# Performance work log

Hardware: AMD Instinct MI355X
Metric: run time of the kernel (lower is better)

The kernel has to match this reference:

```python
import jax, jax.numpy as jnp
import numpy as np

N = 1024  # feature_size == hidden_size == n_nodes
K = 3     # diffusion hops
B = 2048  # batch


def setup_inputs() -> dict:
    key = jax.random.key(0)
    ks = jax.random.split(key, 32)

    # --- adjacency -> normalized K-hop filter list (constants in torch, requires_grad=False) ---
    A = jax.random.uniform(ks[0], (N, N), dtype=jnp.float32) + jnp.eye(N, dtype=jnp.float32)
    # D_inverse = diag(1/sum(A, 0)); norm_A = D_inverse @ A  -> row i scaled by 1/colsum[i]
    norm_A = A / jnp.sum(A, axis=0)[:, None]
    A_temp = jnp.eye(N, dtype=jnp.float32)
    hops = []
    for _ in range(K):
        A_temp = jnp.minimum(A_temp @ norm_A, 1.0)  # Clamp_A: clamp(max=1.0)
        hops.append(A_temp)
    A_list = jnp.stack(hops)  # [K, N, N]

    stdv = 1.0 / np.sqrt(N)
    gin = K * N + 2 * N  # gc_input_size + hidden*2
    rin = N + 2 * N      # input_size + hidden*2

    def U(k, shape, fan_in):
        s = 1.0 / np.sqrt(fan_in)
        return jax.random.uniform(k, shape, jnp.float32, -s, s)

    inp = {
        "input": jax.random.normal(ks[1], (B, N), jnp.float32),
        "input_t": jax.random.normal(ks[2], (B, N), jnp.float32),
        "Hidden_State": jax.random.normal(ks[3], (B, N), jnp.float32),
        "Cell_State": jax.random.normal(ks[4], (B, N), jnp.float32),
        "rHidden_State": jax.random.normal(ks[5], (B, N), jnp.float32),
        "rCell_State": jax.random.normal(ks[6], (B, N), jnp.float32),
        "pred": jax.random.normal(ks[7], (B, N), jnp.float32),
        "A_list": A_list,
        "gc_W": U(ks[8], (K, N, N), N),  # FilterLinear weights (masked by A_list)
        "fl_W": U(ks[9], (N, gin), gin), "fl_b": U(ks[10], (N,), gin),
        "il_W": U(ks[11], (N, gin), gin), "il_b": U(ks[12], (N,), gin),
        "ol_W": U(ks[13], (N, gin), gin), "ol_b": U(ks[14], (N,), gin),
        "Cl_W": U(ks[15], (N, gin), gin), "Cl_b": U(ks[16], (N,), gin),
        "Neighbor_weight": jax.random.uniform(ks[17], (N,), jnp.float32, -stdv, stdv),
        "rfl_W": U(ks[18], (N, rin), rin), "rfl_b": U(ks[19], (N,), rin),
        "ril_W": U(ks[20], (N, rin), rin), "ril_b": U(ks[21], (N,), rin),
        "rol_W": U(ks[22], (N, rin), rin), "rol_b": U(ks[23], (N,), rin),
        "rCl_W": U(ks[24], (N, rin), rin), "rCl_b": U(ks[25], (N,), rin),
        "c": jnp.ones((1,), jnp.float32),
    }
    return inp


def reference(input, input_t, Hidden_State, Cell_State, rHidden_State, rCell_State, pred,
              A_list, gc_W, fl_W, fl_b, il_W, il_b, ol_W, ol_b, Cl_W, Cl_b,
              Neighbor_weight, rfl_W, rfl_b, ril_W, ril_b, rol_W, rol_b, rCl_W, rCl_b, c):
    # K-hop masked graph convolutions: gc_k = x @ (A_k * W_k)^T, concatenated -> [B, K*N]
    gc = jnp.einsum('bn,kmn->bkm', input, A_list * gc_W).reshape(B, K * N)

    combined = jnp.concatenate([gc, Hidden_State, pred], axis=1)  # [B, K*N + 2N]
    f = jax.nn.sigmoid(combined @ fl_W.T + fl_b)
    i = jax.nn.sigmoid(combined @ il_W.T + il_b)
    o = jax.nn.sigmoid(combined @ ol_W.T + ol_b)
    C = jnp.tanh(combined @ Cl_W.T + Cl_b)

    # NC = Cell_State * (A_list[-1] @ Neighbor_weight), broadcast over batch
    NC = Cell_State * (A_list[-1] @ Neighbor_weight)
    Cell = f * NC + i * C
    Hidden = o * jnp.tanh(Cell)

    rcombined = jnp.concatenate([input_t, rHidden_State, pred], axis=1)  # [B, 3N]
    rf = jax.nn.sigmoid(rcombined @ rfl_W.T + rfl_b)
    ri = jax.nn.sigmoid(rcombined @ ril_W.T + ril_b)
    ro = jax.nn.sigmoid(rcombined @ rol_W.T + rol_b)
    rC = jnp.tanh(rcombined @ rCl_W.T + rCl_b)
    rCell = rf * rCell_State + ri * rC
    rHidden = ro * jnp.tanh(rCell)

    # torch.var is unbiased (ddof=1)
    var1 = jnp.var(input_t[:, :N], ddof=1)
    var2 = jnp.var(gc, ddof=1)
    pred_new = (Hidden * var1 * c + rHidden[:, :N] * var2) / (var1 + var2 * c)

    Hidden_out = Hidden - pred_new
    # rHidden has exactly N columns, so rHidden[:, N:] is empty -> just subtract
    rHidden_out = rHidden - pred_new
    return (Hidden_out, Cell, gc, rHidden_out, rCell, pred_new)
```

## Files before the change

### kernel.cpp

```cpp
#include <hip/hip_runtime.h>
#include <cstdint>
#include <cstddef>

typedef unsigned short u16;
typedef __attribute__((ext_vector_type(8))) __bf16 bf16x8;
typedef __attribute__((ext_vector_type(4))) float f32x4;

#define DEV __device__ __forceinline__

DEV u16 f2bf(float f) {
  unsigned u = __float_as_uint(f);
  return (u16)((u + 0x7FFFu + ((u >> 16) & 1u)) >> 16);
}
DEV float bf2f(u16 b) { return __uint_as_float((unsigned)b << 16); }

DEV void glds16(const void* g, void* l) {
  __builtin_amdgcn_global_load_lds((const __attribute__((address_space(1))) void*)g,
                                   (__attribute__((address_space(3))) void*)l,
                                   16, 0, 0);
}

#define PREP_GRID 13088

__global__ void prep_all(
    const float* __restrict__ input, const float* __restrict__ input_t,
    const float* __restrict__ HS, const float* __restrict__ rHS,
    const float* __restrict__ pred, const float* __restrict__ A_list,
    const float* __restrict__ gc_W,
    const float* __restrict__ fl_W, const float* __restrict__ il_W,
    const float* __restrict__ ol_W, const float* __restrict__ Cl_W,
    const float* __restrict__ rfl_W, const float* __restrict__ ril_W,
    const float* __restrict__ rol_W, const float* __restrict__ rCl_W,
    const float* __restrict__ fl_b, const float* __restrict__ il_b,
    const float* __restrict__ ol_b, const float* __restrict__ Cl_b,
    const float* __restrict__ rfl_b, const float* __restrict__ ril_b,
    const float* __restrict__ rol_b, const float* __restrict__ rCl_b,
    const float* __restrict__ Nw,
    u16* __restrict__ bA, u16* __restrict__ comb, u16* __restrict__ rcomb,
    u16* __restrict__ AW, u16* __restrict__ gW, u16* __restrict__ rW,
    float* __restrict__ bias_g, float* __restrict__ bias_r,
    float* __restrict__ nvec, float* __restrict__ part1) {
  __shared__ float red[16];
  const int bid = blockIdx.x, tid = threadIdx.x;

  if (bid < 512) {
    for (int i = bid * 256 + tid; i < 524288; i += 131072) {
      float4 v = *(const float4*)(input + (size_t)i * 4);
      *(ushort4*)(bA + (size_t)i * 4) =
          make_ushort4(f2bf(v.x), f2bf(v.y), f2bf(v.z), f2bf(v.w));
    }
  } else if (bid < 2560) {
    int b = bid - 512;
    int j = tid << 2;
    float4 v = *(const float4*)(input_t + (size_t)b * 1024 + j);
    *(ushort4*)(rcomb + (size_t)b * 3072 + j) =
        make_ushort4(f2bf(v.x), f2bf(v.y), f2bf(v.z), f2bf(v.w));
    float ls = v.x + v.y + v.z + v.w;
    float lq = v.x * v.x + v.y * v.y + v.z * v.z + v.w * v.w;
#pragma unroll
    for (int off = 32; off; off >>= 1) { ls += __shfl_down(ls, off); lq += __shfl_down(lq, off); }
    if ((tid & 63) == 0) { int w = tid >> 6; red[w] = ls; red[8 + w] = lq; }
    __syncthreads();
    if (tid == 0) {
      part1[(size_t)b * 2]     = red[0] + red[1] + red[2] + red[3];
      part1[(size_t)b * 2 + 1] = red[8] + red[9] + red[10] + red[11];
    }
  } else if (bid < 3072) {
    for (int i = (bid - 2560) * 256 + tid; i < 524288; i += 131072) {
      int b = i >> 8, j = (i & 255) << 2;
      float4 v = *(const float4*)(HS + (size_t)b * 1024 + j);
      *(ushort4*)(comb + (size_t)b * 5120 + 3072 + j) =
          make_ushort4(f2bf(v.x), f2bf(v.y), f2bf(v.z), f2bf(v.w));
    }
  } else if (bid < 3584) {
    for (int i = (bid - 3072) * 256 + tid; i < 524288; i += 131072) {
      int b = i >> 8, j = (i & 255) << 2;
      float4 v = *(const float4*)(rHS + (size_t)b * 1024 + j);
      *(ushort4*)(rcomb + (size_t)b * 3072 + 1024 + j) =
          make_ushort4(f2bf(v.x), f2bf(v.y), f2bf(v.z), f2bf(v.w));
    }
  } else if (bid < 4096) {
    for (int i = (bid - 3584) * 256 + tid; i < 524288; i += 131072) {
      int b = i >> 8, j = (i & 255) << 2;
      float4 v = *(const float4*)(pred + (size_t)b * 1024 + j);
      ushort4 u = make_ushort4(f2bf(v.x), f2bf(v.y), f2bf(v.z), f2bf(v.w));
      *(ushort4*)(comb + (size_t)b * 5120 + 4096 + j) = u;
      *(ushort4*)(rcomb + (size_t)b * 3072 + 2048 + j) = u;
    }
  } else if (bid < 4864) {
    for (long i = (long)(bid - 4096) * 256 + tid; i < 786432; i += 768L * 256) {
      float4 va = *(const float4*)(A_list + i * 4);
      float4 vw = *(const float4*)(gc_W + i * 4);
      *(ushort4*)(AW + i * 4) = make_ushort4(f2bf(va.x * vw.x), f2bf(va.y * vw.y),
                                             f2bf(va.z * vw.z), f2bf(va.w * vw.w));
    }
  } else if (bid < 8960) {
    int q = bid - 4864;
    int seg = q >> 10, tb = q & 1023;
    const float* s = (seg == 0) ? fl_W : (seg == 1) ? il_W : (seg == 2) ? ol_W : Cl_W;
    u16* dd = gW + (size_t)seg * 5242880;
    for (long i = (long)tb * 256 + tid; i < 1310720; i += 1024L * 256) {
      float4 v = *(const float4*)(s + i * 4);
      *(ushort4*)(dd + i * 4) = make_ushort4(f2bf(v.x), f2bf(v.y), f2bf(v.z), f2bf(v.w));
    }
  } else if (bid < 12032) {
    int q = bid - 8960;
    int seg = q / 768, tb = q - seg * 768;
    const float* s = (seg == 0) ? rfl_W : (seg == 1) ? ril_W : (seg == 2) ? rol_W : rCl_W;
    u16* dd = rW + (size_t)seg * 3145728;
    for (long i = (long)tb * 256 + tid; i < 786432; i += 768L * 256) {
      float4 v = *(const float4*)(s + i * 4);
      *(ushort4*)(dd + i * 4) = make_ushort4(f2bf(v.x), f2bf(v.y), f2bf(v.z), f2bf(v.w));
    }
  } else if (bid < 12064) {
    int i = (bid - 12032) * 256 + tid;
    int seg = i >> 10;
    const float* s = (seg == 0) ? fl_b : (seg == 1) ? il_b : (seg == 2) ? ol_b : (seg == 3) ? Cl_b
                   : (seg == 4) ? rfl_b : (seg == 5) ? ril_b : (seg == 6) ? rol_b : rCl_b;
    float v = s[i & 1023];
    if (i < 4096) bias_g[i] = v; else bias_r[i - 4096] = v;
  } else {
    int m = bid - 12064;
    const float* A3 = A_list + 2L * 1024 * 1024;
    float s = 0.f;
    for (int c = tid; c < 1024; c += 256) s += A3[(size_t)m * 1024 + c] * Nw[c];
#pragma unroll
    for (int off = 32; off; off >>= 1) s += __shfl_down(s, off);
    if ((tid & 63) == 0) red[tid >> 6] = s;
    __syncthreads();
    if (tid == 0) nvec[m] = red[0] + red[1] + red[2] + red[3];
  }
}

__global__ void reduce_sums(const float* __restrict__ p1, int n1,
                            const float* __restrict__ p2, int n2,
                            float* __restrict__ sums) {
  float a = 0.f, b = 0.f, c = 0.f, d = 0.f;
  for (int i = threadIdx.x; i < n1; i += 256) { a += p1[2 * i]; b += p1[2 * i + 1]; }
  for (int i = threadIdx.x; i < n2; i += 256) { c += p2[2 * i]; d += p2[2 * i + 1]; }
#pragma unroll
  for (int off = 32; off; off >>= 1) {
    a += __shfl_down(a, off); b += __shfl_down(b, off);
    c += __shfl_down(c, off); d += __shfl_down(d, off);
  }
  __shared__ float red[16];
  if ((threadIdx.x & 63) == 0) {
    int w = threadIdx.x >> 6;
    red[w] = a; red[4 + w] = b; red[8 + w] = c; red[12 + w] = d;
  }
  __syncthreads();
  if (threadIdx.x == 0) {
    sums[0] = red[0] + red[1] + red[2] + red[3];
    sums[1] = red[4] + red[5] + red[6] + red[7];
    sums[2] = red[8] + red[9] + red[10] + red[11];
    sums[3] = red[12] + red[13] + red[14] + red[15];
  }
}

__launch_bounds__(256)
__global__ void gemm_bt(const u16* __restrict__ A, int lda,
                        const u16* __restrict__ W, int ldw, int K,
                        float* __restrict__ out0, int ld0,
                        u16* __restrict__ outb, int ldb,
                        float* __restrict__ partials) {
  __shared__ u16 lA[128 * 64];
  __shared__ u16 lB[128 * 64];
  const int tid = threadIdx.x;
  const int w = tid >> 6, l = tid & 63;
  const int bm = blockIdx.y << 7, bn = blockIdx.x << 7;
  const int waveM = ((w >> 1) & 1) << 6, waveN = (w & 1) << 6;
  const int quad = l >> 4, r16 = l & 15;

  const int srow = l >> 3;
  const int schunk = (l & 7) ^ srow;
  const u16* gA = A + (size_t)(bm + w * 32 + srow) * lda + schunk * 8;
  const u16* gB = W + (size_t)(bn + w * 32 + srow) * ldw + schunk * 8;
  u16* sA = lA + (w * 32) * 64;
  u16* sB = lB + (w * 32) * 64;

  f32x4 acc[4][4] = {};

  for (int k0 = 0; k0 < K; k0 += 64) {
#pragma unroll
    for (int i = 0; i < 4; i++) {
      glds16(gA + (size_t)(i * 8) * lda + k0, sA + i * 8 * 64);
      glds16(gB + (size_t)(i * 8) * ldw + k0, sB + i * 8 * 64);
    }
    __syncthreads();
#pragma unroll
    for (int ks = 0; ks < 2; ks++) {
      bf16x8 av[4], bv[4];
#pragma unroll
      for (int mi = 0; mi < 4; mi++) {
        int row = waveM + mi * 16 + r16;
        int ch = (ks * 4 + quad) ^ (r16 & 7);
        av[mi] = *(const bf16x8*)(lA + row * 64 + ch * 8);
      }
#pragma unroll
      for (int ni = 0; ni < 4; ni++) {
        int row = waveN + ni * 16 + r16;
        int ch = (ks * 4 + quad) ^ (r16 & 7);
        bv[ni] = *(const bf16x8*)(lB + row * 64 + ch * 8);
      }
#pragma unroll
      for (int mi = 0; mi < 4; mi++)
#pragma unroll
        for (int ni = 0; ni < 4; ni++)
          acc[mi][ni] = __builtin_amdgcn_mfma_f32_16x16x32_bf16(av[mi], bv[ni], acc[mi][ni], 0, 0, 0);
    }
    __syncthreads();
  }

  float ls = 0.f, lq = 0.f;
#pragma unroll
  for (int mi = 0; mi < 4; mi++)
#pragma unroll
    for (int ni = 0; ni < 4; ni++) {
      int col = bn + waveN + ni * 16 + r16;
#pragma unroll
      for (int e = 0; e < 4; e++) {
        int row = bm + waveM + mi * 16 + quad * 4 + e;
        float v = acc[mi][ni][e];
        out0[(size_t)row * ld0 + col] = v;
        outb[(size_t)row * ldb + col] = f2bf(v);
        ls += v;
        lq += v * v;
      }
    }
#pragma unroll
  for (int off = 32; off; off >>= 1) { ls += __shfl_down(ls, off); lq += __shfl_down(lq, off); }
  __shared__ float red[8];
  if (l == 0) { red[w] = ls; red[4 + w] = lq; }
  __syncthreads();
  if (tid == 0) {
    int bidx = blockIdx.y * gridDim.x + blockIdx.x;
    partials[(size_t)bidx * 2]     = red[0] + red[1] + red[2] + red[3];
    partials[(size_t)bidx * 2 + 1] = red[4] + red[5] + red[6] + red[7];
  }
}

__launch_bounds__(512, 2)
__global__ void gemm_fused(const u16* __restrict__ comb, const u16* __restrict__ gW,
                           const u16* __restrict__ rcomb, const u16* __restrict__ rW,
                           u16* __restrict__ gp2a, u16* __restrict__ gp2b,
                           u16* __restrict__ gp3) {
  __shared__ __attribute__((aligned(16))) u16 sm[2 * 32768];
  const int tid = threadIdx.x;
  const int w = tid >> 6, l = tid & 63;
  const int quad = l >> 4, r16 = l & 15;
  const int wr = w >> 2, wc = w & 3;
  const int b = blockIdx.x;
  const int h = b & 1, t = b >> 1;
  const int ty = t & 7, tx = t >> 3;
  const int bm = ty << 8, bn = tx << 8;
  const int srow = l >> 3;
  const int schunk = (l & 7) ^ srow;

  f32x4 acc[8][4];

  auto run = [&](const u16* Abase, int lda, const u16* Wbase, int ldw,
                 int kBegin, int NT, u16* outp) {
    const u16* gA = Abase + (size_t)(bm + w * 32 + srow) * lda + schunk * 8 + kBegin;
    const u16* gB = Wbase + (size_t)(bn + w * 32 + srow) * ldw + schunk * 8 + kBegin;
#pragma unroll
    for (int mi = 0; mi < 8; mi++)
#pragma unroll
      for (int ni = 0; ni < 4; ni++) acc[mi][ni] = f32x4{0.f, 0.f, 0.f, 0.f};

    auto stage = [&](int tt, int slot) {
      const size_t k0 = (size_t)tt * 64;
      u16* sA = sm + slot * 32768 + (w * 32) * 64;
      u16* sB = sm + slot * 32768 + 16384 + (w * 32) * 64;
#pragma unroll
      for (int j = 0; j < 4; j++) {
        glds16(gA + (size_t)(j * 8) * lda + k0, sA + j * 8 * 64);
        glds16(gB + (size_t)(j * 8) * ldw + k0, sB + j * 8 * 64);
      }
    };
    auto compute = [&](int slot) {
      const u16* sA = sm + slot * 32768;
      const u16* sB = sA + 16384;
#pragma unroll
      for (int ks = 0; ks < 2; ks++) {
        bf16x8 av[8], bv[4];
#pragma unroll
        for (int mi = 0; mi < 8; mi++) {
          int row = wr * 128 + mi * 16 + r16;
          int ch = (ks * 4 + quad) ^ (r16 & 7);
          av[mi] = *(const bf16x8*)(sA + row * 64 + ch * 8);
        }
#pragma unroll
        for (int ni = 0; ni < 4; ni++) {
          int row = wc * 64 + ni * 16 + r16;
          int ch = (ks * 4 + quad) ^ (r16 & 7);
          bv[ni] = *(const bf16x8*)(sB + row * 64 + ch * 8);
        }
        __builtin_amdgcn_s_setprio(1);
#pragma unroll
        for (int mi = 0; mi < 8; mi++)
#pragma unroll
          for (int ni = 0; ni < 4; ni++)
            acc[mi][ni] = __builtin_amdgcn_mfma_f32_16x16x32_bf16(av[mi], bv[ni], acc[mi][ni], 0, 0, 0);
        __builtin_amdgcn_s_setprio(0);
      }
    };

    stage(0, 0);
#pragma unroll 1
    for (int tt = 0; tt < NT; tt++) {
      stage(tt + 1, (tt + 1) & 1);
      __builtin_amdgcn_sched_barrier(0);
      asm volatile("s_waitcnt vmcnt(8)" ::: "memory");
      __builtin_amdgcn_s_barrier();
      __builtin_amdgcn_sched_barrier(0);
      compute(tt & 1);
      __builtin_amdgcn_s_barrier();
    }
#pragma unroll
    for (int mi = 0; mi < 8; mi++)
#pragma unroll
      for (int ni = 0; ni < 4; ni++) {
        int col = bn + wc * 64 + ni * 16 + r16;
#pragma unroll
        for (int e = 0; e < 4; e++) {
          int row = bm + wr * 128 + mi * 16 + quad * 4 + e;
          outp[(size_t)row * 4096 + col] = f2bf(acc[mi][ni][e]);
        }
      }
    __builtin_amdgcn_sched_barrier(0);
    asm volatile("s_waitcnt vmcnt(0)" ::: "memory");
    __builtin_amdgcn_s_barrier();
  };

  if (h == 0) {
    run(comb, 5120, gW, 5120, 0, 16, gp2a);
    run(rcomb, 3072, rW, 3072, 0, 48, gp3);
  } else {
    run(comb, 5120, gW, 5120, 1024, 64, gp2b);
  }
}


DEV float4 gate2(const u16* __restrict__ p0, const u16* __restrict__ p1,
                 const float* __restrict__ bias, size_t base, int boff) {
  ushort4 a = *(const ushort4*)(p0 + base);
  ushort4 b = *(const ushort4*)(p1 + base);
  float4 bb = *(const float4*)(bias + boff);
  return make_float4(bf2f(a.x) + bf2f(b.x) + bb.x, bf2f(a.y) + bf2f(b.y) + bb.y,
                     bf2f(a.z) + bf2f(b.z) + bb.z, bf2f(a.w) + bf2f(b.w) + bb.w);
}
DEV float4 gate1(const u16* __restrict__ p0, const float* __restrict__ bias,
                 size_t base, int boff) {
  ushort4 a = *(const ushort4*)(p0 + base);
  float4 bb = *(const float4*)(bias + boff);
  return make_float4(bf2f(a.x) + bb.x, bf2f(a.y) + bb.y, bf2f(a.z) + bb.z, bf2f(a.w) + bb.w);
}
DEV float4 sig4(float4 v) {
  return make_float4(1.f / (1.f + __expf(-v.x)), 1.f / (1.f + __expf(-v.y)),
                     1.f / (1.f + __expf(-v.z)), 1.f / (1.f + __expf(-v.w)));
}
DEV float4 tanh4(float4 v) {
  return make_float4(tanhf(v.x), tanhf(v.y), tanhf(v.z), tanhf(v.w));
}

__global__ void epilogue(const u16* __restrict__ gp2a, const u16* __restrict__ gp2b,
                         const u16* __restrict__ gp3,
                         const float* __restrict__ bias_g, const float* __restrict__ bias_r,
                         const float* __restrict__ CS, const float* __restrict__ rCS,
                         const float* __restrict__ nvec,
                         const float* __restrict__ sums, const float* __restrict__ cp,
                         float* __restrict__ Hout, float* __restrict__ CellOut,
                         float* __restrict__ rHout, float* __restrict__ rCellOut,
                         float* __restrict__ predOut) {
  const float n1 = 2097152.f, n2 = 6291456.f;
  float var1 = (sums[1] - sums[0] * sums[0] / n1) / (n1 - 1.f);
  float var2 = (sums[3] - sums[2] * sums[2] / n2) / (n2 - 1.f);
  float c = cp[0];
  float inv = 1.f / (var1 + var2 * c);
  float s1 = var1 * c, s2 = var2;

  int t = blockIdx.x * blockDim.x + threadIdx.x;
  int b = t >> 8, j = (t & 255) << 2;
  size_t rb = (size_t)b * 4096 + j;

  float4 f = sig4(gate2(gp2a, gp2b, bias_g, rb, j));
  float4 ii = sig4(gate2(gp2a, gp2b, bias_g, rb + 1024, 1024 + j));
  float4 o = sig4(gate2(gp2a, gp2b, bias_g, rb + 2048, 2048 + j));
  float4 C = tanh4(gate2(gp2a, gp2b, bias_g, rb + 3072, 3072 + j));
  float4 rf = sig4(gate1(gp3, bias_r, rb, j));
  float4 ri = sig4(gate1(gp3, bias_r, rb + 1024, 1024 + j));
  float4 ro = sig4(gate1(gp3, bias_r, rb + 2048, 2048 + j));
  float4 rC = tanh4(gate1(gp3, bias_r, rb + 3072, 3072 + j));

  float4 cs = *(const float4*)(CS + (size_t)b * 1024 + j);
  float4 rcs = *(const float4*)(rCS + (size_t)b * 1024 + j);
  float4 nv = *(const float4*)(nvec + j);

  float4 cell, hid, rcell, rhid, p, ho, rho;
  cell.x = f.x * (cs.x * nv.x) + ii.x * C.x; hid.x = o.x * tanhf(cell.x);
  cell.y = f.y * (cs.y * nv.y) + ii.y * C.y; hid.y = o.y * tanhf(cell.y);
  cell.z = f.z * (cs.z * nv.z) + ii.z * C.z; hid.z = o.z * tanhf(cell.z);
  cell.w = f.w * (cs.w * nv.w) + ii.w * C.w; hid.w = o.w * tanhf(cell.w);
  rcell.x = rf.x * rcs.x + ri.x * rC.x; rhid.x = ro.x * tanhf(rcell.x);
  rcell.y = rf.y * rcs.y + ri.y * rC.y; rhid.y = ro.y * tanhf(rcell.y);
  rcell.z = rf.z * rcs.z + ri.z * rC.z; rhid.z = ro.z * tanhf(rcell.z);
  rcell.w = rf.w * rcs.w + ri.w * rC.w; rhid.w = ro.w * tanhf(rcell.w);
  p.x = (hid.x * s1 + rhid.x * s2) * inv; ho.x = hid.x - p.x; rho.x = rhid.x - p.x;
  p.y = (hid.y * s1 + rhid.y * s2) * inv; ho.y = hid.y - p.y; rho.y = rhid.y - p.y;
  p.z = (hid.z * s1 + rhid.z * s2) * inv; ho.z = hid.z - p.z; rho.z = rhid.z - p.z;
  p.w = (hid.w * s1 + rhid.w * s2) * inv; ho.w = hid.w - p.w; rho.w = rhid.w - p.w;

  size_t i = (size_t)b * 1024 + j;
  *(float4*)(CellOut + i) = cell;
  *(float4*)(rCellOut + i) = rcell;
  *(float4*)(Hout + i) = ho;
  *(float4*)(rHout + i) = rho;
  *(float4*)(predOut + i) = p;
}


extern "C" void kernel_launch(void* const* d_in, const int* in_sizes, int n_in,
                              void* d_out, int out_size, void* d_ws, size_t ws_size,
                              hipStream_t stream) {
  const float* input   = (const float*)d_in[0];
  const float* input_t = (const float*)d_in[1];
  const float* HS      = (const float*)d_in[2];
  const float* CS      = (const float*)d_in[3];
  const float* rHS     = (const float*)d_in[4];
  const float* rCS     = (const float*)d_in[5];
  const float* pred    = (const float*)d_in[6];
  const float* A_list  = (const float*)d_in[7];
  const float* gc_W    = (const float*)d_in[8];
  const float* fl_W  = (const float*)d_in[9];  const float* fl_b  = (const float*)d_in[10];
  const float* il_W  = (const float*)d_in[11]; const float* il_b  = (const float*)d_in[12];
  const float* ol_W  = (const float*)d_in[13]; const float* ol_b  = (const float*)d_in[14];
  const float* Cl_W  = (const float*)d_in[15]; const float* Cl_b  = (const float*)d_in[16];
  const float* Nw    = (const float*)d_in[17];
  const float* rfl_W = (const float*)d_in[18]; const float* rfl_b = (const float*)d_in[19];
  const float* ril_W = (const float*)d_in[20]; const float* ril_b = (const float*)d_in[21];
  const float* rol_W = (const float*)d_in[22]; const float* rol_b = (const float*)d_in[23];
  const float* rCl_W = (const float*)d_in[24]; const float* rCl_b = (const float*)d_in[25];
  const float* cp    = (const float*)d_in[26];

  float* out      = (float*)d_out;
  float* Hout     = out;
  float* CellOut  = out + 2097152;
  float* gcOut    = out + 4194304;
  float* rHout    = out + 10485760;
  float* rCellOut = out + 12582912;
  float* predOut  = out + 14680064;

  char* ws = (char*)d_ws;
  size_t off = 0;
  auto alloc = [&](size_t bytes) -> void* {
    void* p = ws + off;
    off = (off + bytes + 255) & ~(size_t)255;
    return p;
  };
  float* sums   = (float*)alloc(16);
  float* part1  = (float*)alloc(2048 * 2 * 4);
  float* part2  = (float*)alloc(384 * 2 * 4);
  float* nvec   = (float*)alloc(1024 * 4);
  float* bias_g = (float*)alloc(4096 * 4);
  float* bias_r = (float*)alloc(4096 * 4);
  u16* comb  = (u16*)alloc((size_t)2048 * 5120 * 2);
  u16* rcomb = (u16*)alloc((size_t)2048 * 3072 * 2);
  u16* AW    = (u16*)alloc((size_t)3 * 1024 * 1024 * 2);
  u16* gW    = (u16*)alloc((size_t)4096 * 5120 * 2);
  u16* rW    = (u16*)alloc((size_t)4096 * 3072 * 2);
  u16* gp2a  = (u16*)alloc((size_t)2048 * 4096 * 2);
  u16* gp2b  = (u16*)alloc((size_t)2048 * 4096 * 2);
  u16* gp3   = (u16*)alloc((size_t)2048 * 4096 * 2);
  u16* bA = (u16*)gp2a;

  prep_all<<<PREP_GRID, 256, 0, stream>>>(
      input, input_t, HS, rHS, pred, A_list, gc_W,
      fl_W, il_W, ol_W, Cl_W, rfl_W, ril_W, rol_W, rCl_W,
      fl_b, il_b, ol_b, Cl_b, rfl_b, ril_b, rol_b, rCl_b, Nw,
      bA, comb, rcomb, AW, gW, rW, bias_g, bias_r, nvec, part1);

  gemm_bt<<<dim3(24, 16), 256, 0, stream>>>(bA, 1024, AW, 1024, 1024,
                                            gcOut, 3072, comb, 5120, part2);
  reduce_sums<<<1, 256, 0, stream>>>(part1, 2048, part2, 384, sums);
  gemm_fused<<<256, 512, 0, stream>>>(comb, gW, rcomb, rW, gp2a, gp2b, gp3);
  epilogue<<<2048, 256, 0, stream>>>(gp2a, gp2b, gp3, bias_g, bias_r, CS, rCS, nvec,
                                     sums, cp, Hout, CellOut, rHout, rCellOut, predOut);

  (void)in_sizes; (void)n_in; (void)out_size; (void)ws_size;
}
```

Measured before the change: 461.1 us.

## Restructure GEMM mainloop into quadrant-staged pipeline with interleaved loads and MFMA

```diff
diff --git a/kernel.cpp b/kernel.cpp
--- a/kernel.cpp
+++ b/kernel.cpp
@@ -19,6 +19,11 @@
                                    (__attribute__((address_space(3))) void*)l,
                                    16, 0, 0);
 }
+
+#define BAR() __builtin_amdgcn_s_barrier()
+#define SB() __builtin_amdgcn_sched_barrier(0)
+#define LGK0() asm volatile("s_waitcnt lgkmcnt(0)" ::: "memory")
+#define VM(n) asm volatile("s_waitcnt vmcnt(" #n ")" ::: "memory")
 
 #define PREP_GRID 13088
 
@@ -248,88 +253,149 @@
   const int tid = threadIdx.x;
   const int w = tid >> 6, l = tid & 63;
   const int quad = l >> 4, r16 = l & 15;
-  const int wr = w >> 2, wc = w & 3;
+  const int sr = w >> 1, sc = w & 1;
   const int b = blockIdx.x;
   const int h = b & 1, t = b >> 1;
   const int ty = t & 7, tx = t >> 3;
   const int bm = ty << 8, bn = tx << 8;
-  const int srow = l >> 3;
-  const int schunk = (l & 7) ^ srow;
-
-  f32x4 acc[8][4];
+  const int srow = tid >> 3;
+  const int schunk = (tid & 7) ^ (srow & 7);
 
   auto run = [&](const u16* Abase, int lda, const u16* Wbase, int ldw,
                  int kBegin, int NT, u16* outp) {
-    const u16* gA = Abase + (size_t)(bm + w * 32 + srow) * lda + schunk * 8 + kBegin;
-    const u16* gB = Wbase + (size_t)(bn + w * 32 + srow) * ldw + schunk * 8 + kBegin;
-#pragma unroll
-    for (int mi = 0; mi < 8; mi++)
-#pragma unroll
-      for (int ni = 0; ni < 4; ni++) acc[mi][ni] = f32x4{0.f, 0.f, 0.f, 0.f};
-
-    auto stage = [&](int tt, int slot) {
-      const size_t k0 = (size_t)tt * 64;
-      u16* sA = sm + slot * 32768 + (w * 32) * 64;
-      u16* sB = sm + slot * 32768 + 16384 + (w * 32) * 64;
-#pragma unroll
-      for (int j = 0; j < 4; j++) {
-        glds16(gA + (size_t)(j * 8) * lda + k0, sA + j * 8 * 64);
-        glds16(gB + (size_t)(j * 8) * ldw + k0, sB + j * 8 * 64);
-      }
+    const u16* gA = Abase + (size_t)(bm + srow) * lda + schunk * 8 + kBegin;
+    const u16* gB = Wbase + (size_t)(bn + srow) * ldw + schunk * 8 + kBegin;
+
+    f32x4 acc[2][2][2][4];
+#pragma unroll
+    for (int a = 0; a < 2; a++)
+#pragma unroll
+      for (int c = 0; c < 2; c++)
+#pragma unroll
+        for (int mi = 0; mi < 2; mi++)
+#pragma unroll
+          for (int ni = 0; ni < 4; ni++) acc[a][c][mi][ni] = f32x4{0.f, 0.f, 0.f, 0.f};
+
+    bf16x8 av0[2][2], av1[2][2], bv[4][2];
+
+    auto stageA = [&](int buf, int hA, int T) {
+      const u16* g = gA + (size_t)(hA * 128) * lda + (size_t)T * 64;
+      u16* d = sm + buf * 32768 + hA * 8192 + tid * 8;
+      glds16(g, d);
+      glds16(g + (size_t)64 * lda, d + 4096);
     };
-    auto compute = [&](int slot) {
-      const u16* sA = sm + slot * 32768;
-      const u16* sB = sA + 16384;
-#pragma unroll
-      for (int ks = 0; ks < 2; ks++) {
-        bf16x8 av[8], bv[4];
-#pragma unroll
-        for (int mi = 0; mi < 8; mi++) {
-          int row = wr * 128 + mi * 16 + r16;
+    auto stageB = [&](int buf, int hB, int T) {
+      const u16* g = gB + (size_t)(hB * 128) * ldw + (size_t)T * 64;
+      u16* d = sm + buf * 32768 + 16384 + hB * 8192 + tid * 8;
+      glds16(g, d);
+      glds16(g + (size_t)64 * ldw, d + 4096);
+    };
+    auto rdA = [&](int buf, int qr) {
+      const u16* base = sm + buf * 32768;
+#pragma unroll
+      for (int mi = 0; mi < 2; mi++)
+#pragma unroll
+        for (int ks = 0; ks < 2; ks++) {
+          int row = qr * 128 + sr * 32 + mi * 16 + r16;
           int ch = (ks * 4 + quad) ^ (r16 & 7);
-          av[mi] = *(const bf16x8*)(sA + row * 64 + ch * 8);
+          bf16x8 v = *(const bf16x8*)(base + row * 64 + ch * 8);
+          if (qr) av1[mi][ks] = v; else av0[mi][ks] = v;
         }
-#pragma unroll
-        for (int ni = 0; ni < 4; ni++) {
-          int row = wc * 64 + ni * 16 + r16;
+    };
+    auto rdB = [&](int buf, int qc) {
+      const u16* base = sm + buf * 32768 + 16384;
+#pragma unroll
+      for (int ni = 0; ni < 4; ni++)
+#pragma unroll
+        for (int ks = 0; ks < 2; ks++) {
+          int row = qc * 128 + sc * 64 + ni * 16 + r16;
           int ch = (ks * 4 + quad) ^ (r16 & 7);
-          bv[ni] = *(const bf16x8*)(sB + row * 64 + ch * 8);
+          bv[ni][ks] = *(const bf16x8*)(base + row * 64 + ch * 8);
         }
-        __builtin_amdgcn_s_setprio(1);
-#pragma unroll
-        for (int mi = 0; mi < 8; mi++)
+    };
+    auto mf = [&](int qr, int qc) {
+      __builtin_amdgcn_s_setprio(1);
+#pragma unroll
+      for (int ks = 0; ks < 2; ks++)
+#pragma unroll
+        for (int mi = 0; mi < 2; mi++)
 #pragma unroll
           for (int ni = 0; ni < 4; ni++)
-            acc[mi][ni] = __builtin_amdgcn_mfma_f32_16x16x32_bf16(av[mi], bv[ni], acc[mi][ni], 0, 0, 0);
-        __builtin_amdgcn_s_setprio(0);
-      }
+            acc[qr][qc][mi][ni] = __builtin_amdgcn_mfma_f32_16x16x32_bf16(
+                qr ? av1[mi][ks] : av0[mi][ks], bv[ni][ks], acc[qr][qc][mi][ni], 0, 0, 0);
+      __builtin_amdgcn_s_setprio(0);
     };
 
-    stage(0, 0);
+    stageB(0, 0, 0); stageA(0, 0, 0); stageA(0, 1, 0); stageB(0, 1, 0);
+    stageB(1, 0, 1); stageA(1, 0, 1);
+    SB(); VM(8); BAR(); SB();
+
 #pragma unroll 1
-    for (int tt = 0; tt < NT; tt++) {
-      stage(tt + 1, (tt + 1) & 1);
-      __builtin_amdgcn_sched_barrier(0);
-      asm volatile("s_waitcnt vmcnt(8)" ::: "memory");
-      __builtin_amdgcn_s_barrier();
-      __builtin_amdgcn_sched_barrier(0);
-      compute(tt & 1);
-      __builtin_amdgcn_s_barrier();
-    }
-#pragma unroll
-    for (int mi = 0; mi < 8; mi++)
-#pragma unroll
-      for (int ni = 0; ni < 4; ni++) {
-        int col = bn + wc * 64 + ni * 16 + r16;
-#pragma unroll
-        for (int e = 0; e < 4; e++) {
-          int row = bm + wr * 128 + mi * 16 + quad * 4 + e;
-          outp[(size_t)row * 4096 + col] = f2bf(acc[mi][ni][e]);
-        }
-      }
-    __builtin_amdgcn_sched_barrier(0);
-    asm volatile("s_waitcnt vmcnt(0)" ::: "memory");
-    __builtin_amdgcn_s_barrier();
+    for (int T = 0; T < NT - 2; T++) {
+      const int cur = T & 1, nxt = cur ^ 1;
+      rdA(cur, 0); rdB(cur, 0);
+      stageA(nxt, 1, T + 1);
+      SB(); VM(8); BAR(); SB();
+      LGK0(); SB();
+      mf(0, 0);
+      BAR(); SB();
+      rdA(cur, 1);
+      stageB(nxt, 1, T + 1);
+      SB(); VM(8); BAR(); SB();
+      LGK0(); SB();
+      mf(1, 0);
+      BAR(); SB();
+      rdB(cur, 1);
+      stageB(cur, 0, T + 2);
+      SB(); BAR(); SB();
+      LGK0(); SB();
+      mf(0, 1);
+      BAR(); SB();
+      stageA(cur, 0, T + 2);
+      SB(); VM(8); BAR(); SB();
+      mf(1, 1);
+      BAR(); SB();
+    }
+    {
+      const int cur = (NT - 2) & 1, nxt = cur ^ 1;
+      rdA(cur, 0); rdB(cur, 0);
+      stageA(nxt, 1, NT - 1);
+      SB(); VM(8); BAR(); SB(); LGK0(); SB(); mf(0, 0); BAR(); SB();
+      rdA(cur, 1);
+      stageB(nxt, 1, NT - 1);
+      SB(); VM(8); BAR(); SB(); LGK0(); SB(); mf(1, 0); BAR(); SB();
+      rdB(cur, 1);
+      SB(); BAR(); SB(); LGK0(); SB(); mf(0, 1); BAR(); SB();
+      SB(); VM(4); BAR(); SB(); mf(1, 1); BAR(); SB();
+    }
+    {
+      const int cur = (NT - 1) & 1;
+      rdA(cur, 0); rdB(cur, 0);
+      SB(); VM(2); BAR(); SB(); LGK0(); SB(); mf(0, 0); BAR(); SB();
+      rdA(cur, 1);
+      SB(); VM(0); BAR(); SB(); LGK0(); SB(); mf(1, 0); BAR(); SB();
+      rdB(cur, 1);
+      SB(); BAR(); SB(); LGK0(); SB(); mf(0, 1); BAR(); SB();
+      mf(1, 1);
+      BAR(); SB();
+    }
+
+#pragma unroll
+    for (int qr = 0; qr < 2; qr++)
+#pragma unroll
+      for (int qc = 0; qc < 2; qc++)
+#pragma unroll
+        for (int mi = 0; mi < 2; mi++)
+#pragma unroll
+          for (int ni = 0; ni < 4; ni++) {
+            int col = bn + qc * 128 + sc * 64 + ni * 16 + r16;
+#pragma unroll
+            for (int e = 0; e < 4; e++) {
+              int row = bm + qr * 128 + sr * 32 + mi * 16 + quad * 4 + e;
+              outp[(size_t)row * 4096 + col] = f2bf(acc[qr][qc][mi][ni][e]);
+            }
+          }
+    SB(); VM(0); SB();
   };
 
   if (h == 0) {
```

Result: faster. 444.1 us (-3.7%).
